# Kernel tuning notes

Measured on AMD Instinct MI355X. Metric: run time of the kernel, lower is better.

Reference implementation:

```python
import jax, jax.numpy as jnp
import numpy as np
from jax import lax

B, T = 8192, 128
HID = 64


def setup_inputs() -> dict:
    key = jax.random.key(0)
    ks = jax.random.split(key, 16)
    actor_ids = jax.random.randint(ks[0], (B, T), 0, 7, dtype=jnp.int32)
    action_ids = jax.random.randint(ks[1], (B, T), 0, 4, dtype=jnp.int32)
    street_ids = jax.random.randint(ks[2], (B, T), 0, 5, dtype=jnp.int32)
    bet_fraction = jax.random.uniform(ks[3], (B, T, 1), dtype=jnp.float32)
    # prefix-valid mask from random lengths (some zero-length rows)
    lengths = jax.random.randint(ks[4], (B,), 0, T + 1)
    valid_mask = jnp.arange(T)[None, :] < lengths[:, None]  # [B,T] bool
    s = 0.1
    params = {
        "E_actor": jax.random.normal(ks[5], (7, 8), jnp.float32) * s,
        "E_action": jax.random.normal(ks[6], (4, 8), jnp.float32) * s,
        "E_street": jax.random.normal(ks[7], (5, 4), jnp.float32) * s,
        "W_proj": jax.random.normal(ks[8], (32, 21), jnp.float32) * s,
        "b_proj": jax.random.normal(ks[9], (32,), jnp.float32) * s,
        "W_ih": jax.random.normal(ks[10], (3 * HID, 32), jnp.float32) * s,
        "W_hh": jax.random.normal(ks[11], (3 * HID, HID), jnp.float32) * s,
        "b_ih": jax.random.normal(ks[12], (3 * HID,), jnp.float32) * s,
        "b_hh": jax.random.normal(ks[13], (3 * HID,), jnp.float32) * s,
    }
    return dict(actor_ids=actor_ids, action_ids=action_ids, street_ids=street_ids,
                bet_fraction=bet_fraction, valid_mask=valid_mask, **params)


def reference(actor_ids, action_ids, street_ids, bet_fraction, valid_mask,
              E_actor, E_action, E_street, W_proj, b_proj,
              W_ih, W_hh, b_ih, b_hh):
    # embed + concat -> [B,T,21]
    feats = jnp.concatenate([E_actor[actor_ids], E_action[action_ids],
                             E_street[street_ids], bet_fraction], axis=-1)
    x = feats @ W_proj.T + b_proj                      # [B,T,32]
    # precompute input-side GRU gates for all timesteps: [B,T,3H]
    xg = x @ W_ih.T + b_ih
    xg_t = jnp.swapaxes(xg, 0, 1)                      # [T,B,3H]
    m_t = jnp.swapaxes(valid_mask, 0, 1)               # [T,B]

    def step(h, inp):
        xg_i, m = inp
        hg = h @ W_hh.T + b_hh                         # [B,3H]
        xr, xz, xn = jnp.split(xg_i, 3, axis=-1)
        hr, hz, hn = jnp.split(hg, 3, axis=-1)
        r = jax.nn.sigmoid(xr + hr)
        z = jax.nn.sigmoid(xz + hz)
        n = jnp.tanh(xn + r * hn)
        h_new = (1.0 - z) * n + z * h
        # only advance hidden state while t < length (prefix-valid mask);
        # final carry equals the GRU hidden at the last valid step, and rows
        # with length 0 stay at the zero init (matches torch masking).
        h = jnp.where(m[:, None], h_new, h)
        return h, None

    h0 = jnp.zeros((x.shape[0], HID), dtype=x.dtype)
    h_final, _ = lax.scan(step, h0, (xg_t, m_t))
    return h_final
```

## Files before the change

### kernel.cpp

```cpp
#include <hip/hip_runtime.h>

#define HID 64
#define TT  128
#define NROWS 8192
#define NGRP (NROWS / 16)
#define LOG2E 1.44269504088896f

typedef _Float16 half8 __attribute__((ext_vector_type(8)));
typedef float    f32x4 __attribute__((ext_vector_type(4)));

__global__ __launch_bounds__(256, 2) void gru_fused(
    const int* __restrict__ actor_ids, const int* __restrict__ action_ids,
    const int* __restrict__ street_ids, const float* __restrict__ bet,
    const int* __restrict__ mask,
    const float* __restrict__ E_actor, const float* __restrict__ E_action,
    const float* __restrict__ E_street, const float* __restrict__ W_proj,
    const float* __restrict__ b_proj, const float* __restrict__ W_ih,
    const float* __restrict__ b_ih, const float* __restrict__ W_hh,
    const float* __restrict__ b_hh, float* __restrict__ out)
{
    __shared__ __align__(16) union {
        float wfs[192][32];
        struct {
            int pb[TT][17];
            __align__(16) _Float16 hb[2][16][72];
            int part[16][16];
            int Lsh[16];
        } c;
    } A;
    __shared__ __align__(16) _Float16 embl[144];
    __shared__ float bfs[192];

    const int tid = threadIdx.x;
    const int wv  = tid >> 6;
    const int l   = tid & 63;
    const int q   = l >> 4;
    const int n   = l & 15;
    const int g   = blockIdx.x;

    for (int i = tid; i < 136; i += 256) {
        int r = i >> 3, m = i & 7;
        float v = 0.f;
        if (r < 7)       v = E_actor[r * 8 + m];
        else if (r < 11) v = E_action[(r - 7) * 8 + m];
        else if (r < 16) v = (m < 4) ? E_street[(r - 11) * 4 + m] : 0.f;
        embl[i] = (_Float16)v;
    }

    if (tid < 192) {
        const int j = tid;
        float wf[21];
        #pragma unroll
        for (int m = 0; m < 21; m++) wf[m] = 0.f;
        float bf = b_ih[j];
        for (int k = 0; k < 32; k++) {
            const float w = W_ih[j * 32 + k];
            bf += w * b_proj[k];
            #pragma unroll
            for (int m = 0; m < 21; m++) wf[m] += w * W_proj[k * 21 + m];
        }
        const float s = (j < 128) ? LOG2E : 2.f * LOG2E;
        #pragma unroll
        for (int m = 0; m < 21; m++) A.wfs[j][m] = wf[m] * s;
        #pragma unroll
        for (int m = 21; m < 32; m++) A.wfs[j][m] = 0.f;
        bfs[j] = bf;
    }
    __syncthreads();

    half8 Af[3], Ah[3][2];
    {
        const int m16 = l & 15, kq = l >> 4;
        #pragma unroll
        for (int g3 = 0; g3 < 3; g3++) {
            const int jr = g3 * 64 + wv * 16 + m16;
            _Float16 v[8];
            #pragma unroll
            for (int m = 0; m < 8; m++) v[m] = (_Float16)A.wfs[jr][kq * 8 + m];
            Af[g3] = *(half8*)v;
            const float s = (g3 < 2) ? LOG2E : 2.f * LOG2E;
            #pragma unroll
            for (int kt = 0; kt < 2; kt++) {
                _Float16 w[8];
                #pragma unroll
                for (int m = 0; m < 8; m++)
                    w[m] = (_Float16)(W_hh[jr * HID + kt * 32 + kq * 8 + m] * s);
                Ah[g3][kt] = *(half8*)w;
            }
        }
    }
    f32x4 biasR, biasZ, biasX, biasH;
    #pragma unroll
    for (int e = 0; e < 4; e++) {
        const int idx = 16 * wv + 4 * q + e;
        biasR[e] = (bfs[idx]      + b_hh[idx])      * LOG2E;
        biasZ[e] = (bfs[64 + idx] + b_hh[64 + idx]) * LOG2E;
        biasX[e] = bfs[128 + idx]  * (2.f * LOG2E);
        biasH[e] = b_hh[128 + idx] * (2.f * LOG2E);
    }
    __syncthreads();

    for (int i = tid; i < 2 * 16 * 72 / 2; i += 256) ((int*)A.c.hb)[i] = 0;
    {
        const int r = tid >> 4, tl = tid & 15;
        const int base = (g * 16 + r) * TT;
        int cnt = 0;
        #pragma unroll
        for (int i = 0; i < 8; i++) {
            const int t = tl + 16 * i;
            const int a = actor_ids[base + t], c = action_ids[base + t];
            const int s = street_ids[base + t];
            const _Float16 f16 = (_Float16)bet[base + t];
            const unsigned fb = (unsigned)*(const unsigned short*)&f16;
            A.c.pb[t][r] = (int)(a | (c << 3) | (s << 5) | (fb << 16));
            cnt += (mask[base + t] != 0);
        }
        A.c.part[r][tl] = cnt;
    }
    __syncthreads();
    if (tid < 16) {
        int L = 0;
        #pragma unroll
        for (int i = 0; i < 16; i++) L += A.c.part[tid][i];
        A.c.Lsh[tid] = L;
    }
    __syncthreads();

    const int Ln = A.c.Lsh[n];
    int Lmax = Ln;
    #pragma unroll
    for (int k = 1; k < 16; k <<= 1) {
        const int o = __shfl_xor(Lmax, k);
        Lmax = (o > Lmax) ? o : Lmax;
    }

    const bool isq2 = (q == 2);
    const int sh = (q == 1) ? 3 : (q == 2) ? 5 : 0;
    const int mk = (q == 1) ? 3 : (q == 3) ? 0 : 7;
    const int of = (q == 1) ? 7 : (q == 2) ? 11 : (q == 3) ? 16 : 0;

    float h[4] = {0.f, 0.f, 0.f, 0.f};

    f32x4 xR, xZ, xX;
    {
        const int p = A.c.pb[0][n];
        const int eidx = ((p >> sh) & mk) + of;
        half8 Bf = *(const half8*)&embl[eidx * 8];
        uint4* bu = (uint4*)&Bf;
        bu->z = isq2 ? ((unsigned)p >> 16) : bu->z;
        xR = __builtin_amdgcn_mfma_f32_16x16x32_f16(Af[0], Bf, biasR, 0, 0, 0);
        xZ = __builtin_amdgcn_mfma_f32_16x16x32_f16(Af[1], Bf, biasZ, 0, 0, 0);
        xX = __builtin_amdgcn_mfma_f32_16x16x32_f16(Af[2], Bf, biasX, 0, 0, 0);
    }

    for (int t = 0; t < Lmax; t++) {
        const int buf = t & 1;
        const half8 Bh0 = *(const half8*)&A.c.hb[buf][n][q * 8];
        const half8 Bh1 = *(const half8*)&A.c.hb[buf][n][32 + q * 8];
        f32x4 aR = __builtin_amdgcn_mfma_f32_16x16x32_f16(Ah[0][0], Bh0, xR, 0, 0, 0);
        aR = __builtin_amdgcn_mfma_f32_16x16x32_f16(Ah[0][1], Bh1, aR, 0, 0, 0);
        f32x4 aZ = __builtin_amdgcn_mfma_f32_16x16x32_f16(Ah[1][0], Bh0, xZ, 0, 0, 0);
        aZ = __builtin_amdgcn_mfma_f32_16x16x32_f16(Ah[1][1], Bh1, aZ, 0, 0, 0);
        f32x4 aH = __builtin_amdgcn_mfma_f32_16x16x32_f16(Ah[2][0], Bh0, biasH, 0, 0, 0);
        aH = __builtin_amdgcn_mfma_f32_16x16x32_f16(Ah[2][1], Bh1, aH, 0, 0, 0);
        const f32x4 aXc = xX;

        {
            const int tn = (t + 1 < TT) ? t + 1 : TT - 1;
            const int p = A.c.pb[tn][n];
            const int eidx = ((p >> sh) & mk) + of;
            half8 Bf = *(const half8*)&embl[eidx * 8];
            uint4* bu = (uint4*)&Bf;
            bu->z = isq2 ? ((unsigned)p >> 16) : bu->z;
            xR = __builtin_amdgcn_mfma_f32_16x16x32_f16(Af[0], Bf, biasR, 0, 0, 0);
            xZ = __builtin_amdgcn_mfma_f32_16x16x32_f16(Af[1], Bf, biasZ, 0, 0, 0);
            xX = __builtin_amdgcn_mfma_f32_16x16x32_f16(Af[2], Bf, biasX, 0, 0, 0);
        }

        const bool live = (t < Ln);
        _Float16 hp[4];
        #pragma unroll
        for (int e = 0; e < 4; e++) {
            const float r = __builtin_amdgcn_rcpf(1.f + __builtin_amdgcn_exp2f(-aR[e]));
            const float z = __builtin_amdgcn_rcpf(1.f + __builtin_amdgcn_exp2f(-aZ[e]));
            const float y2 = aXc[e] + r * aH[e];
            const float nn = 1.f - 2.f * __builtin_amdgcn_rcpf(1.f + __builtin_amdgcn_exp2f(y2));
            const float hv = nn + z * (h[e] - nn);
            h[e] = live ? hv : h[e];
            hp[e] = (_Float16)h[e];
        }
        *(uint2*)&A.c.hb[buf ^ 1][n][16 * wv + 4 * q] = *(uint2*)hp;
        __syncthreads();
    }

    float4 o = make_float4(h[0], h[1], h[2], h[3]);
    *(float4*)&out[(g * 16 + n) * HID + 16 * wv + 4 * q] = o;
}

extern "C" void kernel_launch(void* const* d_in, const int* in_sizes, int n_in,
                              void* d_out, int out_size, void* d_ws, size_t ws_size,
                              hipStream_t stream) {
    const int*   actor_ids  = (const int*)d_in[0];
    const int*   action_ids = (const int*)d_in[1];
    const int*   street_ids = (const int*)d_in[2];
    const float* bet        = (const float*)d_in[3];
    const int*   vmask      = (const int*)d_in[4];
    const float* E_actor    = (const float*)d_in[5];
    const float* E_action   = (const float*)d_in[6];
    const float* E_street   = (const float*)d_in[7];
    const float* W_proj     = (const float*)d_in[8];
    const float* b_proj     = (const float*)d_in[9];
    const float* W_ih       = (const float*)d_in[10];
    const float* W_hh       = (const float*)d_in[11];
    const float* b_ih       = (const float*)d_in[12];
    const float* b_hh       = (const float*)d_in[13];
    float*       out        = (float*)d_out;

    gru_fused<<<NGRP, 256, 0, stream>>>(actor_ids, action_ids, street_ids, bet,
                                        vmask, E_actor, E_action, E_street,
                                        W_proj, b_proj, W_ih, b_ih, W_hh, b_hh,
                                        out);
}
```

Measured before the change: 168.2 us.

## Sort rows by sequence length so GRU blocks share similar loop trip counts

Adds three pre-kernels that compute per-row valid lengths, build a length histogram with a prefix sum, and counting-sort rows into a permutation. Each block of 16 rows then holds rows of similar length, so the per-block loop bound (max length in the group) wastes fewer masked steps. Long and short groups are interleaved in the block mapping so the two blocks per CU get balanced work. The cost is four extra launches plus a memset, and gathered row loads and scattered output stores.

```diff
diff --git a/kernel.cpp b/kernel.cpp
--- a/kernel.cpp
+++ b/kernel.cpp
@@ -9,23 +9,53 @@
 typedef _Float16 half8 __attribute__((ext_vector_type(8)));
 typedef float    f32x4 __attribute__((ext_vector_type(4)));
 
+
+__global__ void k_len(const int* __restrict__ mask, int* __restrict__ lens,
+                      int* __restrict__ hist) {
+    const int row = blockIdx.x * 4 + (threadIdx.x >> 6);
+    const int l   = threadIdx.x & 63;
+    const int* mrow = mask + row * TT;
+    int c = (mrow[l] != 0) + (mrow[l + 64] != 0);
+    #pragma unroll
+    for (int k = 32; k >= 1; k >>= 1) c += __shfl_xor(c, k);
+    if (l == 0) { lens[row] = c; atomicAdd(&hist[c], 1); }
+}
+
+__global__ void k_prefix(const int* __restrict__ hist, int* __restrict__ offs) {
+    if (threadIdx.x == 0) {
+        int s = 0;
+        for (int i = 0; i <= TT; i++) { offs[i] = s; s += hist[i]; }
+    }
+}
+
+__global__ void k_scatter(const int* __restrict__ lens, int* __restrict__ offs,
+                          int* __restrict__ perm) {
+    const int row = blockIdx.x * 256 + threadIdx.x;
+    const int L   = lens[row];
+    const int pos = atomicAdd(&offs[L], 1);
+    const int d   = NROWS - 1 - pos;
+    const int gd  = d >> 4, r = d & 15;
+    const int b   = (gd < 256) ? gd : 767 - gd;
+    perm[b * 16 + r] = row;
+}
+
 __global__ __launch_bounds__(256, 2) void gru_fused(
     const int* __restrict__ actor_ids, const int* __restrict__ action_ids,
     const int* __restrict__ street_ids, const float* __restrict__ bet,
-    const int* __restrict__ mask,
     const float* __restrict__ E_actor, const float* __restrict__ E_action,
     const float* __restrict__ E_street, const float* __restrict__ W_proj,
     const float* __restrict__ b_proj, const float* __restrict__ W_ih,
     const float* __restrict__ b_ih, const float* __restrict__ W_hh,
-    const float* __restrict__ b_hh, float* __restrict__ out)
+    const float* __restrict__ b_hh, const int* __restrict__ perm,
+    const int* __restrict__ lens, float* __restrict__ out)
 {
     __shared__ __align__(16) union {
         float wfs[192][32];
         struct {
             int pb[TT][17];
             __align__(16) _Float16 hb[2][16][72];
-            int part[16][16];
             int Lsh[16];
+            int Psh[16];
         } c;
     } A;
     __shared__ __align__(16) _Float16 embl[144];
@@ -103,8 +133,8 @@
     for (int i = tid; i < 2 * 16 * 72 / 2; i += 256) ((int*)A.c.hb)[i] = 0;
     {
         const int r = tid >> 4, tl = tid & 15;
-        const int base = (g * 16 + r) * TT;
-        int cnt = 0;
+        const int prow = perm[g * 16 + r];
+        const int base = prow * TT;
         #pragma unroll
         for (int i = 0; i < 8; i++) {
             const int t = tl + 16 * i;
@@ -113,16 +143,8 @@
             const _Float16 f16 = (_Float16)bet[base + t];
             const unsigned fb = (unsigned)*(const unsigned short*)&f16;
             A.c.pb[t][r] = (int)(a | (c << 3) | (s << 5) | (fb << 16));
-            cnt += (mask[base + t] != 0);
-        }
-        A.c.part[r][tl] = cnt;
-    }
-    __syncthreads();
-    if (tid < 16) {
-        int L = 0;
-        #pragma unroll
-        for (int i = 0; i < 16; i++) L += A.c.part[tid][i];
-        A.c.Lsh[tid] = L;
+        }
+        if (tl == 0) { A.c.Lsh[r] = lens[prow]; A.c.Psh[r] = prow; }
     }
     __syncthreads();
 
@@ -193,8 +215,9 @@
         __syncthreads();
     }
 
+    const int prow = A.c.Psh[n];
     float4 o = make_float4(h[0], h[1], h[2], h[3]);
-    *(float4*)&out[(g * 16 + n) * HID + 16 * wv + 4 * q] = o;
+    *(float4*)&out[prow * HID + 16 * wv + 4 * q] = o;
 }
 
 extern "C" void kernel_launch(void* const* d_in, const int* in_sizes, int n_in,
@@ -216,8 +239,19 @@
     const float* b_hh       = (const float*)d_in[13];
     float*       out        = (float*)d_out;
 
+    int* ws   = (int*)d_ws;
+    int* lens = ws;
+    int* perm = ws + NROWS;
+    int* hist = ws + 2 * NROWS;
+    int* offs = ws + 2 * NROWS + 160;
+
+    hipMemsetAsync(hist, 0, (TT + 1) * sizeof(int), stream);
+    k_len<<<NROWS / 4, 256, 0, stream>>>(vmask, lens, hist);
+    k_prefix<<<1, 64, 0, stream>>>(hist, offs);
+    k_scatter<<<NROWS / 256, 256, 0, stream>>>(lens, offs, perm);
+
     gru_fused<<<NGRP, 256, 0, stream>>>(actor_ids, action_ids, street_ids, bet,
-                                        vmask, E_actor, E_action, E_street,
+                                        E_actor, E_action, E_street,
                                         W_proj, b_proj, W_ih, b_ih, W_hh, b_hh,
-                                        out);
-}
+                                        perm, lens, out);
+}
```

Result: slower. 195.5 us (+16.2%).

## Make each wave own eight rows end-to-end to drop per-step block barriers

Applied to the files above, without the earlier changes.

Each wavefront now computes all 192 gate rows for its own 8 sequences, so the hidden state stays in wave-private LDS. This removes the __syncthreads at every timestep. The input-side bias is folded into the fused weight through a constant-one feature, and the input projection is recomputed inside the step loop instead of being prefetched. Sequence lengths are reduced with shuffles, and each wave's loop bound is the max length over its 8 rows. In exchange, half of each 16-column MFMA is spent on duplicated columns, so there are more MFMAs per row. Blocks now cover 32 rows with launch bounds of 1, which lowers the number of resident waves available to hide the serial recurrence latency.

```diff
diff --git a/kernel.cpp b/kernel.cpp
--- a/kernel.cpp
+++ b/kernel.cpp
@@ -3,13 +3,13 @@
 #define HID 64
 #define TT  128
 #define NROWS 8192
-#define NGRP (NROWS / 16)
+#define NBLK (NROWS / 32)
 #define LOG2E 1.44269504088896f
 
 typedef _Float16 half8 __attribute__((ext_vector_type(8)));
 typedef float    f32x4 __attribute__((ext_vector_type(4)));
 
-__global__ __launch_bounds__(256, 2) void gru_fused(
+__global__ __launch_bounds__(256, 1) void gru_fused(
     const int* __restrict__ actor_ids, const int* __restrict__ action_ids,
     const int* __restrict__ street_ids, const float* __restrict__ bet,
     const int* __restrict__ mask,
@@ -22,20 +22,19 @@
     __shared__ __align__(16) union {
         float wfs[192][32];
         struct {
-            int pb[TT][17];
-            __align__(16) _Float16 hb[2][16][72];
-            int part[16][16];
-            int Lsh[16];
+            int pb[TT][33];
+            __align__(16) _Float16 hbuf[4][8][80];
         } c;
     } A;
     __shared__ __align__(16) _Float16 embl[144];
-    __shared__ float bfs[192];
 
     const int tid = threadIdx.x;
-    const int wv  = tid >> 6;
+    const int w   = tid >> 6;
     const int l   = tid & 63;
-    const int q   = l >> 4;
-    const int n   = l & 15;
+    const int u   = l >> 4;
+    const int c   = l & 15;
+    const int cr  = c & 7;
+    const bool loT = (c < 8);
     const int g   = blockIdx.x;
 
     for (int i = tid; i < 136; i += 256) {
@@ -49,152 +48,172 @@
 
     if (tid < 192) {
         const int j = tid;
-        float wf[21];
-        #pragma unroll
-        for (int m = 0; m < 21; m++) wf[m] = 0.f;
+        float wf[22];
+        #pragma unroll
+        for (int m = 0; m < 22; m++) wf[m] = 0.f;
         float bf = b_ih[j];
         for (int k = 0; k < 32; k++) {
-            const float w = W_ih[j * 32 + k];
-            bf += w * b_proj[k];
+            const float wv = W_ih[j * 32 + k];
+            bf += wv * b_proj[k];
             #pragma unroll
-            for (int m = 0; m < 21; m++) wf[m] += w * W_proj[k * 21 + m];
-        }
+            for (int m = 0; m < 21; m++) wf[m] += wv * W_proj[k * 21 + m];
+        }
+        wf[21] = bf + (j < 128 ? b_hh[j] : 0.f);
         const float s = (j < 128) ? LOG2E : 2.f * LOG2E;
         #pragma unroll
-        for (int m = 0; m < 21; m++) A.wfs[j][m] = wf[m] * s;
-        #pragma unroll
-        for (int m = 21; m < 32; m++) A.wfs[j][m] = 0.f;
-        bfs[j] = bf;
+        for (int m = 0; m < 22; m++) A.wfs[j][m] = wf[m] * s;
+        #pragma unroll
+        for (int m = 22; m < 32; m++) A.wfs[j][m] = 0.f;
     }
     __syncthreads();
 
-    half8 Af[3], Ah[3][2];
+    half8 Af[12], Ah[12][2];
+    #pragma unroll
+    for (int jt = 0; jt < 12; jt++) {
+        const int jr = jt * 16 + c;
+        _Float16 v[8];
+        #pragma unroll
+        for (int m = 0; m < 8; m++) v[m] = (_Float16)A.wfs[jr][u * 8 + m];
+        Af[jt] = *(half8*)v;
+        const float s = (jt < 8) ? LOG2E : 2.f * LOG2E;
+        #pragma unroll
+        for (int kt = 0; kt < 2; kt++) {
+            _Float16 w8[8];
+            #pragma unroll
+            for (int m = 0; m < 8; m++)
+                w8[m] = (_Float16)(W_hh[jr * HID + kt * 32 + u * 8 + m] * s);
+            Ah[jt][kt] = *(half8*)w8;
+        }
+    }
+    f32x4 biasH[4];
+    #pragma unroll
+    for (int T = 0; T < 4; T++)
+        #pragma unroll
+        for (int e = 0; e < 4; e++)
+            biasH[T][e] = b_hh[128 + 16 * T + 4 * u + e] * (2.f * LOG2E);
+    __syncthreads();
+
+    int Lrow;
     {
-        const int m16 = l & 15, kq = l >> 4;
-        #pragma unroll
-        for (int g3 = 0; g3 < 3; g3++) {
-            const int jr = g3 * 64 + wv * 16 + m16;
-            _Float16 v[8];
-            #pragma unroll
-            for (int m = 0; m < 8; m++) v[m] = (_Float16)A.wfs[jr][kq * 8 + m];
-            Af[g3] = *(half8*)v;
-            const float s = (g3 < 2) ? LOG2E : 2.f * LOG2E;
-            #pragma unroll
-            for (int kt = 0; kt < 2; kt++) {
-                _Float16 w[8];
-                #pragma unroll
-                for (int m = 0; m < 8; m++)
-                    w[m] = (_Float16)(W_hh[jr * HID + kt * 32 + kq * 8 + m] * s);
-                Ah[g3][kt] = *(half8*)w;
-            }
-        }
-    }
-    f32x4 biasR, biasZ, biasX, biasH;
-    #pragma unroll
-    for (int e = 0; e < 4; e++) {
-        const int idx = 16 * wv + 4 * q + e;
-        biasR[e] = (bfs[idx]      + b_hh[idx])      * LOG2E;
-        biasZ[e] = (bfs[64 + idx] + b_hh[64 + idx]) * LOG2E;
-        biasX[e] = bfs[128 + idx]  * (2.f * LOG2E);
-        biasH[e] = b_hh[128 + idx] * (2.f * LOG2E);
-    }
-    __syncthreads();
-
-    for (int i = tid; i < 2 * 16 * 72 / 2; i += 256) ((int*)A.c.hb)[i] = 0;
+        const int r32 = tid >> 3, j = tid & 7;
+        const int base = (g * 32 + r32) * TT;
+        int cnt = 0;
+        #pragma unroll
+        for (int i = 0; i < 16; i++) {
+            const int t = j + 8 * i;
+            const int a = actor_ids[base + t], ac = action_ids[base + t];
+            const int s = street_ids[base + t];
+            const _Float16 f16v = (_Float16)bet[base + t];
+            const unsigned fb = (unsigned)*(const unsigned short*)&f16v;
+            A.c.pb[t][r32] = (int)(a | (ac << 3) | (s << 5) | (fb << 16));
+            cnt += (mask[base + t] != 0);
+        }
+        cnt += __shfl_xor(cnt, 1);
+        cnt += __shfl_xor(cnt, 2);
+        cnt += __shfl_xor(cnt, 4);
+        Lrow = cnt;
+    }
+    const int Ln = __shfl(Lrow, cr << 3);
+    int Lmax = Ln;
+    { int o = __shfl_xor(Lmax, 1); Lmax = o > Lmax ? o : Lmax; }
+    { int o = __shfl_xor(Lmax, 2); Lmax = o > Lmax ? o : Lmax; }
+    { int o = __shfl_xor(Lmax, 4); Lmax = o > Lmax ? o : Lmax; }
+
+    _Float16* hbW = &A.c.hbuf[w][cr][0];
+    const int T0f = loT ? 0 : 32;
     {
-        const int r = tid >> 4, tl = tid & 15;
-        const int base = (g * 16 + r) * TT;
-        int cnt = 0;
-        #pragma unroll
-        for (int i = 0; i < 8; i++) {
-            const int t = tl + 16 * i;
-            const int a = actor_ids[base + t], c = action_ids[base + t];
-            const int s = street_ids[base + t];
-            const _Float16 f16 = (_Float16)bet[base + t];
-            const unsigned fb = (unsigned)*(const unsigned short*)&f16;
-            A.c.pb[t][r] = (int)(a | (c << 3) | (s << 5) | (fb << 16));
-            cnt += (mask[base + t] != 0);
-        }
-        A.c.part[r][tl] = cnt;
-    }
-    __syncthreads();
-    if (tid < 16) {
-        int L = 0;
-        #pragma unroll
-        for (int i = 0; i < 16; i++) L += A.c.part[tid][i];
-        A.c.Lsh[tid] = L;
-    }
-    __syncthreads();
-
-    const int Ln = A.c.Lsh[n];
-    int Lmax = Ln;
-    #pragma unroll
-    for (int k = 1; k < 16; k <<= 1) {
-        const int o = __shfl_xor(Lmax, k);
-        Lmax = (o > Lmax) ? o : Lmax;
-    }
-
-    const bool isq2 = (q == 2);
-    const int sh = (q == 1) ? 3 : (q == 2) ? 5 : 0;
-    const int mk = (q == 1) ? 3 : (q == 3) ? 0 : 7;
-    const int of = (q == 1) ? 7 : (q == 2) ? 11 : (q == 3) ? 16 : 0;
-
-    float h[4] = {0.f, 0.f, 0.f, 0.f};
-
-    f32x4 xR, xZ, xX;
+        uint2 z2; z2.x = 0; z2.y = 0;
+        *(uint2*)&hbW[T0f + 4 * u] = z2;
+        *(uint2*)&hbW[T0f + 16 + 4 * u] = z2;
+    }
+
+    const int sh = (u == 1) ? 3 : (u == 2) ? 5 : 0;
+    const int mk = (u == 1) ? 3 : (u == 3) ? 0 : 7;
+    const int of = (u == 1) ? 7 : (u == 2) ? 11 : (u == 3) ? 16 : 0;
+    const bool isu2 = (u == 2);
+
+    const f32x4 zero4 = {0.f, 0.f, 0.f, 0.f};
+    float hA[4] = {0.f, 0.f, 0.f, 0.f}, hB[4] = {0.f, 0.f, 0.f, 0.f};
+
+    half8 Bf;
     {
-        const int p = A.c.pb[0][n];
-        const int eidx = ((p >> sh) & mk) + of;
-        half8 Bf = *(const half8*)&embl[eidx * 8];
+        const int p = A.c.pb[0][8 * w + cr];
+        Bf = *(const half8*)&embl[(((p >> sh) & mk) + of) * 8];
         uint4* bu = (uint4*)&Bf;
-        bu->z = isq2 ? ((unsigned)p >> 16) : bu->z;
-        xR = __builtin_amdgcn_mfma_f32_16x16x32_f16(Af[0], Bf, biasR, 0, 0, 0);
-        xZ = __builtin_amdgcn_mfma_f32_16x16x32_f16(Af[1], Bf, biasZ, 0, 0, 0);
-        xX = __builtin_amdgcn_mfma_f32_16x16x32_f16(Af[2], Bf, biasX, 0, 0, 0);
+        bu->z = isu2 ? (((unsigned)p >> 16) | 0x3C000000u) : bu->z;
     }
 
     for (int t = 0; t < Lmax; t++) {
-        const int buf = t & 1;
-        const half8 Bh0 = *(const half8*)&A.c.hb[buf][n][q * 8];
-        const half8 Bh1 = *(const half8*)&A.c.hb[buf][n][32 + q * 8];
-        f32x4 aR = __builtin_amdgcn_mfma_f32_16x16x32_f16(Ah[0][0], Bh0, xR, 0, 0, 0);
-        aR = __builtin_amdgcn_mfma_f32_16x16x32_f16(Ah[0][1], Bh1, aR, 0, 0, 0);
-        f32x4 aZ = __builtin_amdgcn_mfma_f32_16x16x32_f16(Ah[1][0], Bh0, xZ, 0, 0, 0);
-        aZ = __builtin_amdgcn_mfma_f32_16x16x32_f16(Ah[1][1], Bh1, aZ, 0, 0, 0);
-        f32x4 aH = __builtin_amdgcn_mfma_f32_16x16x32_f16(Ah[2][0], Bh0, biasH, 0, 0, 0);
-        aH = __builtin_amdgcn_mfma_f32_16x16x32_f16(Ah[2][1], Bh1, aH, 0, 0, 0);
-        const f32x4 aXc = xX;
-
+        const half8 Bh0 = *(const half8*)&hbW[8 * u];
+        const half8 Bh1 = *(const half8*)&hbW[32 + 8 * u];
+
+        f32x4 x[12];
+        #pragma unroll
+        for (int jt = 0; jt < 12; jt++)
+            x[jt] = __builtin_amdgcn_mfma_f32_16x16x32_f16(Af[jt], Bf, zero4, 0, 0, 0);
+        f32x4 acc[8];
+        #pragma unroll
+        for (int jt = 0; jt < 8; jt++) {
+            f32x4 t0 = __builtin_amdgcn_mfma_f32_16x16x32_f16(Ah[jt][0], Bh0, x[jt], 0, 0, 0);
+            acc[jt]  = __builtin_amdgcn_mfma_f32_16x16x32_f16(Ah[jt][1], Bh1, t0, 0, 0, 0);
+        }
+        f32x4 hn[4];
+        #pragma unroll
+        for (int T = 0; T < 4; T++) {
+            f32x4 t0 = __builtin_amdgcn_mfma_f32_16x16x32_f16(Ah[8 + T][0], Bh0, biasH[T], 0, 0, 0);
+            hn[T]    = __builtin_amdgcn_mfma_f32_16x16x32_f16(Ah[8 + T][1], Bh1, t0, 0, 0, 0);
+        }
+
+        half8 BfN;
         {
             const int tn = (t + 1 < TT) ? t + 1 : TT - 1;
-            const int p = A.c.pb[tn][n];
-            const int eidx = ((p >> sh) & mk) + of;
-            half8 Bf = *(const half8*)&embl[eidx * 8];
-            uint4* bu = (uint4*)&Bf;
-            bu->z = isq2 ? ((unsigned)p >> 16) : bu->z;
-            xR = __builtin_amdgcn_mfma_f32_16x16x32_f16(Af[0], Bf, biasR, 0, 0, 0);
-            xZ = __builtin_amdgcn_mfma_f32_16x16x32_f16(Af[1], Bf, biasZ, 0, 0, 0);
-            xX = __builtin_amdgcn_mfma_f32_16x16x32_f16(Af[2], Bf, biasX, 0, 0, 0);
-        }
+            const int p = A.c.pb[tn][8 * w + cr];
+            BfN = *(const half8*)&embl[(((p >> sh) & mk) + of) * 8];
+            uint4* bu = (uint4*)&BfN;
+            bu->z = isu2 ? (((unsigned)p >> 16) | 0x3C000000u) : bu->z;
+        }
+
+        const f32x4 aRA = loT ? acc[0] : acc[2];
+        const f32x4 aRB = loT ? acc[1] : acc[3];
+        const f32x4 aZA = loT ? acc[4] : acc[6];
+        const f32x4 aZB = loT ? acc[5] : acc[7];
+        const f32x4 hnA = loT ? hn[0] : hn[2];
+        const f32x4 hnB = loT ? hn[1] : hn[3];
+        const f32x4 xnA = loT ? x[8] : x[10];
+        const f32x4 xnB = loT ? x[9] : x[11];
 
         const bool live = (t < Ln);
-        _Float16 hp[4];
+        _Float16 hpA[4], hpB[4];
         #pragma unroll
         for (int e = 0; e < 4; e++) {
-            const float r = __builtin_amdgcn_rcpf(1.f + __builtin_amdgcn_exp2f(-aR[e]));
-            const float z = __builtin_amdgcn_rcpf(1.f + __builtin_amdgcn_exp2f(-aZ[e]));
-            const float y2 = aXc[e] + r * aH[e];
-            const float nn = 1.f - 2.f * __builtin_amdgcn_rcpf(1.f + __builtin_amdgcn_exp2f(y2));
-            const float hv = nn + z * (h[e] - nn);
-            h[e] = live ? hv : h[e];
-            hp[e] = (_Float16)h[e];
-        }
-        *(uint2*)&A.c.hb[buf ^ 1][n][16 * wv + 4 * q] = *(uint2*)hp;
-        __syncthreads();
-    }
-
-    float4 o = make_float4(h[0], h[1], h[2], h[3]);
-    *(float4*)&out[(g * 16 + n) * HID + 16 * wv + 4 * q] = o;
+            {
+                const float r = __builtin_amdgcn_rcpf(1.f + __builtin_amdgcn_exp2f(-aRA[e]));
+                const float z = __builtin_amdgcn_rcpf(1.f + __builtin_amdgcn_exp2f(-aZA[e]));
+                const float y2 = xnA[e] + r * hnA[e];
+                const float nn = 1.f - 2.f * __builtin_amdgcn_rcpf(1.f + __builtin_amdgcn_exp2f(y2));
+                const float hv = nn + z * (hA[e] - nn);
+                hA[e] = live ? hv : hA[e];
+                hpA[e] = (_Float16)hA[e];
+            }
+            {
+                const float r = __builtin_amdgcn_rcpf(1.f + __builtin_amdgcn_exp2f(-aRB[e]));
+                const float z = __builtin_amdgcn_rcpf(1.f + __builtin_amdgcn_exp2f(-aZB[e]));
+                const float y2 = xnB[e] + r * hnB[e];
+                const float nn = 1.f - 2.f * __builtin_amdgcn_rcpf(1.f + __builtin_amdgcn_exp2f(y2));
+                const float hv = nn + z * (hB[e] - nn);
+                hB[e] = live ? hv : hB[e];
+                hpB[e] = (_Float16)hB[e];
+            }
+        }
+        *(uint2*)&hbW[T0f + 4 * u] = *(uint2*)hpA;
+        *(uint2*)&hbW[T0f + 16 + 4 * u] = *(uint2*)hpB;
+
+        Bf = BfN;
+    }
+
+    const int row = g * 32 + 8 * w + cr;
+    *(float4*)&out[row * HID + T0f + 4 * u] = make_float4(hA[0], hA[1], hA[2], hA[3]);
+    *(float4*)&out[row * HID + T0f + 16 + 4 * u] = make_float4(hB[0], hB[1], hB[2], hB[3]);
 }
 
 extern "C" void kernel_launch(void* const* d_in, const int* in_sizes, int n_in,
@@ -216,7 +235,7 @@
     const float* b_hh       = (const float*)d_in[13];
     float*       out        = (float*)d_out;
 
-    gru_fused<<<NGRP, 256, 0, stream>>>(actor_ids, action_ids, street_ids, bet,
+    gru_fused<<<NBLK, 256, 0, stream>>>(actor_ids, action_ids, street_ids, bet,
                                         vmask, E_actor, E_action, E_street,
                                         W_proj, b_proj, W_ih, b_ih, W_hh, b_hh,
                                         out);
```

New measurement: 219.3 us. 30.4% more time.
